# Kernel tuning notes

Hardware: AMD Instinct MI355X
Metric: run time of the kernel (lower is better)

The kernel has to match this reference:

```python
import jax, jax.numpy as jnp
import numpy as np

B, S, D, H = 2, 2048, 1024, 16
HD = D // H
DI = int(8 / 3 * D)  # 2730
EPS = 1e-5


def rmsnorm(x, gamma):
    rms = jnp.sqrt(jnp.mean(x * x, axis=-1, keepdims=True) + EPS)
    return (x / rms) * gamma


def rope(x):
    # x: [B, H, S, HD]; rotate interleaved even/odd pairs, concat halves
    hd = x.shape[-1]
    seq = x.shape[2]
    theta = 1.0 / (10000.0 ** (jnp.arange(0, hd, 2, dtype=jnp.float32) / hd))  # [HD/2]
    ang = jnp.arange(seq, dtype=jnp.float32)[:, None] * theta  # [S, HD/2]
    cos = jnp.cos(ang)[None, None]  # [1,1,S,HD/2]
    sin = jnp.sin(ang)[None, None]
    x1, x2 = x[..., ::2], x[..., 1::2]
    return jnp.concatenate([x1 * cos - x2 * sin, x1 * sin + x2 * cos], axis=-1)


def setup_inputs() -> dict:
    key = jax.random.key(0)
    ks = jax.random.split(key, 8)
    w = lambda k, shape: (jax.random.normal(k, shape, jnp.float32) * 0.02)
    return {
        "x": jax.random.normal(ks[0], (B, S, D), jnp.float32),
        "mask": jnp.tril(jnp.ones((1, 1, S, S), jnp.int32)),  # causal
        "gamma_attn": jnp.ones((D,), jnp.float32),
        "w_qkv": w(ks[1], (3 * D, D)),
        "b_qkv": jnp.zeros((3 * D,), jnp.float32),
        "w_out": w(ks[2], (D, D)),
        "b_out": jnp.zeros((D,), jnp.float32),
        "gamma_ffn": jnp.ones((D,), jnp.float32),
        "w1": w(ks[3], (DI, D)),
        "b1": jnp.zeros((DI,), jnp.float32),
        "w2": w(ks[4], (DI, D)),
        "b2": jnp.zeros((DI,), jnp.float32),
        "w3": w(ks[5], (D, DI)),
        "b3": jnp.zeros((D,), jnp.float32),
    }


def reference(x, mask, gamma_attn, w_qkv, b_qkv, w_out, b_out,
              gamma_ffn, w1, b1, w2, b2, w3, b3):
    batch, seq, d_model = x.shape
    # --- attn norm (pre-norm; residual uses normalized x, matching source) ---
    xn = rmsnorm(x, gamma_attn)
    # --- MHA ---
    qkv = xn @ w_qkv.T + b_qkv  # [B,S,3D]
    q, k, v = jnp.split(qkv, 3, axis=-1)
    q = q.reshape(batch, seq, H, HD).transpose(0, 2, 1, 3)  # [B,H,S,HD]
    k = k.reshape(batch, seq, H, HD).transpose(0, 2, 1, 3)
    v = v.reshape(batch, seq, H, HD).transpose(0, 2, 1, 3)
    q = rope(q)
    k = rope(k)
    scores = jnp.einsum("bhqd,bhkd->bhqk", q, k) / jnp.sqrt(jnp.float32(HD))
    scores = jnp.where(mask == 0, jnp.float32(-jnp.inf), scores)
    attn = jax.nn.softmax(scores, axis=-1)
    out = jnp.einsum("bhqk,bhkd->bhqd", attn, v)
    out = out.transpose(0, 2, 1, 3).reshape(batch, seq, d_model)
    attn_out = out @ w_out.T + b_out
    h = xn + attn_out
    # --- FFN norm + SwiGLU ---
    hn = rmsnorm(h, gamma_ffn)
    gate = jax.nn.silu(hn @ w2.T + b2)
    ff = (hn @ w1.T + b1) * gate
    ffn_out = ff @ w3.T + b3
    return hn + ffn_out
```

## Files before the change

### kernel.cpp

```cpp
#include <hip/hip_runtime.h>

typedef unsigned short u16;
typedef unsigned int u32;
typedef __attribute__((ext_vector_type(8))) short short8;
typedef __attribute__((ext_vector_type(4))) float f32x4;

#define Bt 2
#define St 2048
#define Dm 1024
#define Ht 16
#define HD 64
#define DI 2730
#define DIP 2816
#define DIP2 5632
#define Mrows 4096

typedef const __attribute__((address_space(1))) unsigned char* gp_t;
typedef __attribute__((address_space(3))) unsigned char* lp_t;
#define GLDS16(g, l) __builtin_amdgcn_global_load_lds((gp_t)(g), (lp_t)(l), 16, 0, 0)

__device__ __forceinline__ float bf2f(u16 b){
  union { float f; u32 i; } v; v.i = ((u32)b) << 16; return v.f;
}
__device__ __forceinline__ u16 f2bf(float f){
  union { float f; u32 i; } v; v.f = f;
  u32 u = v.i;
  return (u16)((u + 0x7FFFu + ((u >> 16) & 1u)) >> 16);
}

__global__ __launch_bounds__(256) void prep_k(const float* __restrict__ w_qkv,
                                              const float* __restrict__ w_out,
                                              const float* __restrict__ w1,
                                              const float* __restrict__ w2,
                                              const float* __restrict__ w3,
                                              const float* __restrict__ b1,
                                              const float* __restrict__ b2,
                                              const float* __restrict__ x,
                                              const float* __restrict__ gamma,
                                              u16* __restrict__ w_qkvb,
                                              u16* __restrict__ w_outb,
                                              u16* __restrict__ w12i,
                                              u16* __restrict__ w3b,
                                              float* __restrict__ b12i,
                                              u16* __restrict__ xn)
{
  __shared__ float red[4];
  int bidx = blockIdx.x;
  const int t = threadIdx.x;
  if (bidx < 12288){ const int idx = bidx * 256 + t; w_qkvb[idx] = f2bf(w_qkv[idx]); return; }
  bidx -= 12288;
  if (bidx < 4096){ const int idx = bidx * 256 + t; w_outb[idx] = f2bf(w_out[idx]); return; }
  bidx -= 4096;
  if (bidx < 11264){
    const int idx = bidx * 256 + t;
    const int k = idx >> 10, c = idx & 1023;
    w12i[((size_t)(2 * k)) * 1024 + c] = (k < DI) ? f2bf(w1[idx]) : (u16)0;
    return;
  }
  bidx -= 11264;
  if (bidx < 11264){
    const int idx = bidx * 256 + t;
    const int k = idx >> 10, c = idx & 1023;
    w12i[((size_t)(2 * k + 1)) * 1024 + c] = (k < DI) ? f2bf(w2[idx]) : (u16)0;
    return;
  }
  bidx -= 11264;
  if (bidx < 11264){
    const int idx = bidx * 256 + t;
    const int k = idx % DIP, n = idx / DIP;
    w3b[idx] = (k < DI) ? f2bf(w3[(size_t)n * DI + k]) : (u16)0;
    return;
  }
  bidx -= 11264;
  if (bidx < 22){
    const int idx = bidx * 256 + t;
    if (idx < DIP2){
      const int k = idx >> 1;
      b12i[idx] = (k < DI) ? ((idx & 1) ? b2[k] : b1[k]) : 0.0f;
    }
    return;
  }
  bidx -= 22;
  {
    const size_t base = (size_t)bidx * Dm + t * 4;
    float4 v = *(const float4*)(x + base);
    float ss = v.x*v.x + v.y*v.y + v.z*v.z + v.w*v.w;
    #pragma unroll
    for (int sh = 1; sh < 64; sh <<= 1) ss += __shfl_xor(ss, sh, 64);
    if ((t & 63) == 0) red[t >> 6] = ss;
    __syncthreads();
    float tot = red[0] + red[1] + red[2] + red[3];
    float rinv = 1.0f / sqrtf(tot * (1.0f / 1024.0f) + 1e-5f);
    float4 gv = *(const float4*)(gamma + t * 4);
    uint2 outp;
    outp.x = (u32)f2bf(v.x * rinv * gv.x) | ((u32)f2bf(v.y * rinv * gv.y) << 16);
    outp.y = (u32)f2bf(v.z * rinv * gv.z) | ((u32)f2bf(v.w * rinv * gv.w) << 16);
    *(uint2*)(xn + base) = outp;
  }
}

__global__ __launch_bounds__(256) void rmsnorm2_k(const u16* xa,
                                                  const u16* __restrict__ xb,
                                                  const float* __restrict__ g,
                                                  u16* o)
{
  __shared__ float red[4];
  const int row = blockIdx.x, t = threadIdx.x;
  const size_t base = (size_t)row * Dm + t * 4;
  uint2 va = *(const uint2*)(xa + base);
  uint2 vb = *(const uint2*)(xb + base);
  float f0 = bf2f((u16)(va.x & 0xffff)) + bf2f((u16)(vb.x & 0xffff));
  float f1 = bf2f((u16)(va.x >> 16))    + bf2f((u16)(vb.x >> 16));
  float f2 = bf2f((u16)(va.y & 0xffff)) + bf2f((u16)(vb.y & 0xffff));
  float f3 = bf2f((u16)(va.y >> 16))    + bf2f((u16)(vb.y >> 16));
  float ss = f0*f0 + f1*f1 + f2*f2 + f3*f3;
  #pragma unroll
  for (int sh = 1; sh < 64; sh <<= 1) ss += __shfl_xor(ss, sh, 64);
  if ((t & 63) == 0) red[t >> 6] = ss;
  __syncthreads();
  float tot = red[0] + red[1] + red[2] + red[3];
  float rinv = 1.0f / sqrtf(tot * (1.0f / 1024.0f) + 1e-5f);
  float4 gv = *(const float4*)(g + t * 4);
  uint2 outp;
  outp.x = (u32)f2bf(f0 * rinv * gv.x) | ((u32)f2bf(f1 * rinv * gv.y) << 16);
  outp.y = (u32)f2bf(f2 * rinv * gv.z) | ((u32)f2bf(f3 * rinv * gv.w) << 16);
  *(uint2*)(o + base) = outp;
}

#define BK 32
template<int RES, int WF>
__global__ __launch_bounds__(256) void gemm_bt(const u16* __restrict__ A,
                                               const u16* __restrict__ Bw,
                                               const float* __restrict__ bias,
                                               const u16* __restrict__ res,
                                               void* __restrict__ Cv,
                                               int N, int K, int lda, int ldc)
{
  __shared__ __align__(16) u16 lA[128 * BK];
  __shared__ __align__(16) u16 lB[128 * BK];
  const int tid = threadIdx.x;
  const int m0 = blockIdx.x * 128;
  const int n0 = blockIdx.y * 128;
  const int wave = tid >> 6, lane = tid & 63;
  const int wm = (wave >> 1) * 64, wn = (wave & 1) * 64;
  const int lm = lane & 15, lq = lane >> 4;

  f32x4 acc[4][4] = {};
  const int rl = lane >> 2, seg = lane & 3;

  const int nk = K / BK;
  for (int kt = 0; kt < nk; ++kt){
    const int k0 = kt * BK;
    __syncthreads();
    #pragma unroll
    for (int i = 0; i < 2; ++i){
      const int ra = wave * 32 + i * 16 + rl;
      const int kc = seg ^ ((ra >> 1) & 3);
      GLDS16(A  + (size_t)(m0 + ra) * lda + k0 + kc * 8, &lA[(wave * 32 + i * 16) * BK]);
      GLDS16(Bw + (size_t)(n0 + ra) * K   + k0 + kc * 8, &lB[(wave * 32 + i * 16) * BK]);
    }
    __syncthreads();
    short8 af[4], bfr[4];
    #pragma unroll
    for (int i = 0; i < 4; ++i){
      int r = wm + i * 16 + lm;
      af[i] = *(const short8*)&lA[r * BK + ((lq ^ ((r >> 1) & 3)) * 8)];
    }
    #pragma unroll
    for (int j = 0; j < 4; ++j){
      int r = wn + j * 16 + lm;
      bfr[j] = *(const short8*)&lB[r * BK + ((lq ^ ((r >> 1) & 3)) * 8)];
    }
    #pragma unroll
    for (int i = 0; i < 4; ++i)
      #pragma unroll
      for (int j = 0; j < 4; ++j)
        acc[i][j] = __builtin_amdgcn_mfma_f32_16x16x32_bf16(af[i], bfr[j], acc[i][j], 0, 0, 0);
  }

  #pragma unroll
  for (int i = 0; i < 4; ++i){
    const int row = m0 + wm + i * 16 + lq * 4;
    #pragma unroll
    for (int j = 0; j < 4; ++j){
      const int col = n0 + wn + j * 16 + lm;
      const float bb = bias[col];
      #pragma unroll
      for (int r = 0; r < 4; ++r){
        float v = acc[i][j][r] + bb;
        if (RES) v += bf2f(res[(size_t)(row + r) * ldc + col]);
        if (WF) ((float*)Cv)[(size_t)(row + r) * ldc + col] = v;
        else    ((u16*)Cv)[(size_t)(row + r) * ldc + col] = f2bf(v);
      }
    }
  }
}

__global__ __launch_bounds__(256) void gemm_ffn(const u16* __restrict__ A,
                                                const u16* __restrict__ Bw,
                                                const float* __restrict__ bias,
                                                u16* __restrict__ ff)
{
  __shared__ __align__(16) u16 lA[128 * BK];
  __shared__ __align__(16) u16 lB[128 * BK];
  const int tid = threadIdx.x;
  const int m0 = blockIdx.x * 128;
  const int n0 = blockIdx.y * 128;
  const int wave = tid >> 6, lane = tid & 63;
  const int wm = (wave >> 1) * 64, wn = (wave & 1) * 64;
  const int lm = lane & 15, lq = lane >> 4;

  f32x4 acc[4][4] = {};
  const int rl = lane >> 2, seg = lane & 3;

  for (int kt = 0; kt < 1024 / BK; ++kt){
    const int k0 = kt * BK;
    __syncthreads();
    #pragma unroll
    for (int i = 0; i < 2; ++i){
      const int ra = wave * 32 + i * 16 + rl;
      const int kc = seg ^ ((ra >> 1) & 3);
      GLDS16(A  + (size_t)(m0 + ra) * 1024 + k0 + kc * 8, &lA[(wave * 32 + i * 16) * BK]);
      GLDS16(Bw + (size_t)(n0 + ra) * 1024 + k0 + kc * 8, &lB[(wave * 32 + i * 16) * BK]);
    }
    __syncthreads();
    short8 af[4], bfr[4];
    #pragma unroll
    for (int i = 0; i < 4; ++i){
      int r = wm + i * 16 + lm;
      af[i] = *(const short8*)&lA[r * BK + ((lq ^ ((r >> 1) & 3)) * 8)];
    }
    #pragma unroll
    for (int j = 0; j < 4; ++j){
      int r = wn + j * 16 + lm;
      bfr[j] = *(const short8*)&lB[r * BK + ((lq ^ ((r >> 1) & 3)) * 8)];
    }
    #pragma unroll
    for (int i = 0; i < 4; ++i)
      #pragma unroll
      for (int j = 0; j < 4; ++j)
        acc[i][j] = __builtin_amdgcn_mfma_f32_16x16x32_bf16(af[i], bfr[j], acc[i][j], 0, 0, 0);
  }

  #pragma unroll
  for (int i = 0; i < 4; ++i){
    const int row = m0 + wm + i * 16 + lq * 4;
    #pragma unroll
    for (int j = 0; j < 4; ++j){
      const int col = n0 + wn + j * 16 + lm;
      const float bb = bias[col];
      const int kcol = col >> 1;
      #pragma unroll
      for (int r = 0; r < 4; ++r){
        float v = acc[i][j][r] + bb;
        float g = __shfl_xor(v, 1, 64);
        if ((lm & 1) == 0){
          float ffv = v * (g / (1.0f + __expf(-g)));
          ff[(size_t)(row + r) * DIP + kcol] = f2bf(ffv);
        }
      }
    }
  }
}

template<int RES, int WF>
__global__ __launch_bounds__(256) void gemm_bt64(const u16* __restrict__ A,
                                                 const u16* __restrict__ Bw,
                                                 const float* __restrict__ bias,
                                                 const u16* __restrict__ res,
                                                 void* __restrict__ Cv,
                                                 int N, int K, int lda, int ldc)
{
  __shared__ __align__(16) u16 lA[128 * BK];
  __shared__ __align__(16) u16 lB[64 * BK];
  const int tid = threadIdx.x;
  const int m0 = blockIdx.x * 128;
  const int n0 = blockIdx.y * 64;
  const int wave = tid >> 6, lane = tid & 63;
  const int wm = wave * 32;
  const int lm = lane & 15, lq = lane >> 4;

  f32x4 acc[2][4] = {};
  const int rl = lane >> 2, seg = lane & 3;

  const int nk = K / BK;
  for (int kt = 0; kt < nk; ++kt){
    const int k0 = kt * BK;
    __syncthreads();
    #pragma unroll
    for (int i = 0; i < 2; ++i){
      const int ra = wave * 32 + i * 16 + rl;
      const int kc = seg ^ ((ra >> 1) & 3);
      GLDS16(A + (size_t)(m0 + ra) * lda + k0 + kc * 8, &lA[(wave * 32 + i * 16) * BK]);
    }
    {
      const int rb = wave * 16 + rl;
      const int kc = seg ^ ((rb >> 1) & 3);
      GLDS16(Bw + (size_t)(n0 + rb) * K + k0 + kc * 8, &lB[(wave * 16) * BK]);
    }
    __syncthreads();
    short8 af[2], bfr[4];
    #pragma unroll
    for (int i = 0; i < 2; ++i){
      int r = wm + i * 16 + lm;
      af[i] = *(const short8*)&lA[r * BK + ((lq ^ ((r >> 1) & 3)) * 8)];
    }
    #pragma unroll
    for (int j = 0; j < 4; ++j){
      int r = j * 16 + lm;
      bfr[j] = *(const short8*)&lB[r * BK + ((lq ^ ((r >> 1) & 3)) * 8)];
    }
    #pragma unroll
    for (int i = 0; i < 2; ++i)
      #pragma unroll
      for (int j = 0; j < 4; ++j)
        acc[i][j] = __builtin_amdgcn_mfma_f32_16x16x32_bf16(af[i], bfr[j], acc[i][j], 0, 0, 0);
  }

  #pragma unroll
  for (int i = 0; i < 2; ++i){
    const int row = m0 + wm + i * 16 + lq * 4;
    #pragma unroll
    for (int j = 0; j < 4; ++j){
      const int col = n0 + j * 16 + lm;
      const float bb = bias[col];
      #pragma unroll
      for (int r = 0; r < 4; ++r){
        float v = acc[i][j][r] + bb;
        if (RES) v += bf2f(res[(size_t)(row + r) * ldc + col]);
        if (WF) ((float*)Cv)[(size_t)(row + r) * ldc + col] = v;
        else    ((u16*)Cv)[(size_t)(row + r) * ldc + col] = f2bf(v);
      }
    }
  }
}

__global__ __launch_bounds__(256) void rv_k(const u16* __restrict__ qkv,
                                            u16* __restrict__ qr,
                                            u16* __restrict__ kr,
                                            u16* __restrict__ vT)
{
  __shared__ u16 tbuf[64][66];
  const int bid = blockIdx.x;
  const int tid = threadIdx.x;
  if (bid < 16384){
    const int g = bid * 4 + (tid >> 6);
    const int d = tid & 63;
    const int h = g & 15, m = g >> 4;
    const int s = m & (St - 1), b = m >> 11;
    const int p = d & 31, hi = d >> 5;
    const float theta = __expf(-(float)p * 0.28782313662425575f);
    const float ang = (float)s * theta;
    const float c = cosf(ang), sn = sinf(ang);
    const u16* base = qkv + (size_t)m * 3072;
    float x1q = bf2f(base[h * 64 + 2 * p]);
    float x2q = bf2f(base[h * 64 + 2 * p + 1]);
    float x1k = bf2f(base[1024 + h * 64 + 2 * p]);
    float x2k = bf2f(base[1024 + h * 64 + 2 * p + 1]);
    float vq = (hi == 0) ? (x1q * c - x2q * sn) : (x1q * sn + x2q * c);
    float vk = (hi == 0) ? (x1k * c - x2k * sn) : (x1k * sn + x2k * c);
    const size_t oidx = ((size_t)(b * 16 + h) * St + s) * 64 + d;
    qr[oidx] = f2bf(vq * 0.125f);
    kr[oidx] = f2bf(vk);
  } else {
    const int vt = bid - 16384;
    const int st = vt & 31, bh = vt >> 5;
    const int b = bh >> 4, h = bh & 15;
    const int c2 = (tid & 31) * 2, rg = tid >> 5;
    #pragma unroll
    for (int it = 0; it < 8; ++it){
      int row = rg + it * 8;
      u32 v = *(const u32*)&qkv[(size_t)(b * St + st * 64 + row) * 3072 + 2048 + h * 64 + c2];
      *(u32*)&tbuf[row][c2] = v;
    }
    __syncthreads();
    const int sl = tid & 63;
    #pragma unroll
    for (int it = 0; it < 16; ++it){
      int d = (tid >> 6) + it * 4;
      vT[((size_t)bh * 64 + d) * St + st * 64 + sl] = tbuf[sl][d];
    }
  }
}

__global__ __launch_bounds__(256) void fattn_k(const u16* __restrict__ qr,
                                               const u16* __restrict__ kr,
                                               const u16* __restrict__ vT,
                                               u16* __restrict__ ctx)
{
  __shared__ __align__(16) u16 lK[64 * 80];
  __shared__ __align__(16) u16 lV[64 * 80];
  __shared__ __align__(16) u16 pP[4][2][16 * 72];

  const int bid = blockIdx.x;
  const int bh = bid & 31;
  const int jj = 15 - (bid >> 5);
  const int qt0 = jj << 7;
  const int tid = threadIdx.x;
  const int wave = tid >> 6, lane = tid & 63;
  const int lm = lane & 15, lq = lane >> 4;

  const u16* Kb = kr + (size_t)bh * St * 64;
  const u16* Vb = vT + (size_t)bh * 64 * St;
  const u16* Qb = qr + ((size_t)bh * St + qt0 + wave * 32) * 64;

  short8 qf[2][2];
  #pragma unroll
  for (int st = 0; st < 2; ++st){
    qf[st][0] = *(const short8*)&Qb[(st * 16 + lm) * 64 + lq * 8];
    qf[st][1] = *(const short8*)&Qb[(st * 16 + lm) * 64 + 32 + lq * 8];
  }

  f32x4 o[2][4] = {};
  float ls[2][4] = {};
  const int kend = qt0 + 128;

  for (int kb = 0; kb < kend; kb += 64){
    __syncthreads();
    #pragma unroll
    for (int p = 0; p < 2; ++p){
      const int idx = p * 256 + tid;
      const int r0 = idx >> 3, seg = idx & 7;
      uint4 kv = *(const uint4*)(Kb + (size_t)(kb + r0) * 64 + seg * 8);
      uint4 vv = *(const uint4*)(Vb + (size_t)r0 * St + kb + seg * 8);
      *(uint4*)&lK[r0 * 80 + seg * 8] = kv;
      *(uint4*)&lV[r0 * 80 + seg * 8] = vv;
    }
    __syncthreads();
    f32x4 sc[2][4];
    #pragma unroll
    for (int nt = 0; nt < 4; ++nt){
      const u16* Krow = &lK[(nt * 16 + lm) * 80];
      short8 kf0 = *(const short8*)&Krow[lq * 8];
      short8 kf1 = *(const short8*)&Krow[32 + lq * 8];
      #pragma unroll
      for (int st = 0; st < 2; ++st){
        f32x4 a = {};
        a = __builtin_amdgcn_mfma_f32_16x16x32_bf16(qf[st][0], kf0, a, 0, 0, 0);
        a = __builtin_amdgcn_mfma_f32_16x16x32_bf16(qf[st][1], kf1, a, 0, 0, 0);
        sc[st][nt] = a;
      }
    }
    #pragma unroll
    for (int st = 0; st < 2; ++st){
      const int minrow = qt0 + wave * 32 + st * 16;
      if (kb + 63 > minrow){
        const int rowb = minrow + lq * 4;
        #pragma unroll
        for (int nt = 0; nt < 4; ++nt){
          const int key = kb + nt * 16 + lm;
          #pragma unroll
          for (int r = 0; r < 4; ++r)
            if (key > rowb + r) sc[st][nt][r] = -1e30f;
        }
      }
    }
    #pragma unroll
    for (int st = 0; st < 2; ++st)
      #pragma unroll
      for (int nt = 0; nt < 4; ++nt)
        #pragma unroll
        for (int r = 0; r < 4; ++r){
          float p = __expf(sc[st][nt][r] - 12.0f);
          ls[st][r] += p;
          pP[wave][st][(lq * 4 + r) * 72 + nt * 16 + lm] = f2bf(p);
        }
    short8 pf[2][2];
    #pragma unroll
    for (int st = 0; st < 2; ++st){
      pf[st][0] = *(const short8*)&pP[wave][st][lm * 72 + lq * 8];
      pf[st][1] = *(const short8*)&pP[wave][st][lm * 72 + 32 + lq * 8];
    }
    #pragma unroll
    for (int ct = 0; ct < 4; ++ct){
      const u16* Vrow = &lV[(ct * 16 + lm) * 80];
      short8 vf0 = *(const short8*)&Vrow[lq * 8];
      short8 vf1 = *(const short8*)&Vrow[32 + lq * 8];
      #pragma unroll
      for (int st = 0; st < 2; ++st){
        o[st][ct] = __builtin_amdgcn_mfma_f32_16x16x32_bf16(pf[st][0], vf0, o[st][ct], 0, 0, 0);
        o[st][ct] = __builtin_amdgcn_mfma_f32_16x16x32_bf16(pf[st][1], vf1, o[st][ct], 0, 0, 0);
      }
    }
  }
  #pragma unroll
  for (int sh = 1; sh < 16; sh <<= 1)
    #pragma unroll
    for (int st = 0; st < 2; ++st)
      #pragma unroll
      for (int r = 0; r < 4; ++r)
        ls[st][r] += __shfl_xor(ls[st][r], sh, 64);
  const int b = bh >> 4, h = bh & 15;
  #pragma unroll
  for (int st = 0; st < 2; ++st)
    #pragma unroll
    for (int r = 0; r < 4; ++r){
      const int s = qt0 + wave * 32 + st * 16 + lq * 4 + r;
      const float inv = 1.0f / ls[st][r];
      #pragma unroll
      for (int ct = 0; ct < 4; ++ct){
        const int d = ct * 16 + lm;
        ctx[((size_t)(b * St + s)) * Dm + h * 64 + d] = f2bf(o[st][ct][r] * inv);
      }
    }
}

extern "C" void kernel_launch(void* const* d_in, const int* in_sizes, int n_in,
                              void* d_out, int out_size, void* d_ws, size_t ws_size,
                              hipStream_t stream) {
  (void)in_sizes; (void)n_in; (void)out_size; (void)ws_size;
  const float* x          = (const float*)d_in[0];
  const float* gamma_attn = (const float*)d_in[2];
  const float* w_qkv      = (const float*)d_in[3];
  const float* b_qkv      = (const float*)d_in[4];
  const float* w_out      = (const float*)d_in[5];
  const float* b_out      = (const float*)d_in[6];
  const float* gamma_ffn  = (const float*)d_in[7];
  const float* w1         = (const float*)d_in[8];
  const float* b1         = (const float*)d_in[9];
  const float* w2         = (const float*)d_in[10];
  const float* b2         = (const float*)d_in[11];
  const float* w3         = (const float*)d_in[12];
  const float* b3         = (const float*)d_in[13];
  float* out = (float*)d_out;
  char* ws = (char*)d_ws;

  u16* w_qkvb  = (u16*)(ws + 0);
  u16* w_outb  = (u16*)(ws + 6291456);
  u16* w12i    = (u16*)(ws + 8388608);
  u16* w3b     = (u16*)(ws + 19922944);
  float* b12i  = (float*)(ws + 25690112);
  u16* xn      = (u16*)(ws + 25712640);
  u16* hn      = xn;
  u16* qkv     = (u16*)(ws + 34101248);
  u16* ctx     = (u16*)(ws + 34101248);
  u16* att     = (u16*)(ws + 42489856);
  u16* ff      = (u16*)(ws + 34101248);
  u16* qr      = (u16*)(ws + 59267072);
  u16* kr      = (u16*)(ws + 67655680);
  u16* vT      = (u16*)(ws + 76044288);

  dim3 blk(256);
  prep_k<<<54294, blk, 0, stream>>>(w_qkv, w_out, w1, w2, w3, b1, b2, x, gamma_attn,
                                    w_qkvb, w_outb, w12i, w3b, b12i, xn);
  gemm_bt<0,0><<<dim3(32, 24), blk, 0, stream>>>(xn, w_qkvb, b_qkv, nullptr, qkv, 3072, 1024, 1024, 3072);
  rv_k<<<17408, blk, 0, stream>>>(qkv, qr, kr, vT);
  fattn_k<<<512, blk, 0, stream>>>(qr, kr, vT, ctx);
  gemm_bt64<0,0><<<dim3(32, 16), blk, 0, stream>>>(ctx, w_outb, b_out, nullptr, att, 1024, 1024, 1024, 1024);
  rmsnorm2_k<<<Mrows, blk, 0, stream>>>(xn, att, gamma_ffn, hn);
  gemm_ffn<<<dim3(32, 44), blk, 0, stream>>>(hn, w12i, b12i, ff);
  gemm_bt64<1,1><<<dim3(32, 16), blk, 0, stream>>>(ff, w3b, b3, hn, out, 1024, DIP, DIP, 1024);
}
```

Before: 397.3 us.

## Double GEMM K-tile to 64 with 8-way swizzle and prefetch attention K/V tiles

All three GEMM kernels move from a K-tile of 32 to 64, which halves the number of barrier pairs per K sweep. The LDS XOR swizzle changes to an 8-chunk pattern, and each loaded tile now feeds two MFMA sub-steps. The attention kernel also prefetches the next K/V tile into registers while the current tile is being computed, so global load latency overlaps with math. The cost is more LDS per block and more registers, which may lower occupancy.

```diff
diff --git a/kernel.cpp b/kernel.cpp
--- a/kernel.cpp
+++ b/kernel.cpp
@@ -127,7 +127,7 @@
   *(uint2*)(o + base) = outp;
 }
 
-#define BK 32
+#define BK 64
 template<int RES, int WF>
 __global__ __launch_bounds__(256) void gemm_bt(const u16* __restrict__ A,
                                                const u16* __restrict__ Bw,
@@ -146,36 +146,39 @@
   const int lm = lane & 15, lq = lane >> 4;
 
   f32x4 acc[4][4] = {};
-  const int rl = lane >> 2, seg = lane & 3;
+  const int rl = lane >> 3, seg = lane & 7;
 
   const int nk = K / BK;
   for (int kt = 0; kt < nk; ++kt){
     const int k0 = kt * BK;
     __syncthreads();
     #pragma unroll
-    for (int i = 0; i < 2; ++i){
-      const int ra = wave * 32 + i * 16 + rl;
-      const int kc = seg ^ ((ra >> 1) & 3);
-      GLDS16(A  + (size_t)(m0 + ra) * lda + k0 + kc * 8, &lA[(wave * 32 + i * 16) * BK]);
-      GLDS16(Bw + (size_t)(n0 + ra) * K   + k0 + kc * 8, &lB[(wave * 32 + i * 16) * BK]);
-    }
-    __syncthreads();
-    short8 af[4], bfr[4];
-    #pragma unroll
     for (int i = 0; i < 4; ++i){
-      int r = wm + i * 16 + lm;
-      af[i] = *(const short8*)&lA[r * BK + ((lq ^ ((r >> 1) & 3)) * 8)];
-    }
-    #pragma unroll
-    for (int j = 0; j < 4; ++j){
-      int r = wn + j * 16 + lm;
-      bfr[j] = *(const short8*)&lB[r * BK + ((lq ^ ((r >> 1) & 3)) * 8)];
-    }
-    #pragma unroll
-    for (int i = 0; i < 4; ++i)
-      #pragma unroll
-      for (int j = 0; j < 4; ++j)
-        acc[i][j] = __builtin_amdgcn_mfma_f32_16x16x32_bf16(af[i], bfr[j], acc[i][j], 0, 0, 0);
+      const int ra = wave * 32 + i * 8 + rl;
+      const int kc = seg ^ (ra & 7);
+      GLDS16(A  + (size_t)(m0 + ra) * lda + k0 + kc * 8, &lA[(wave * 32 + i * 8) * BK]);
+      GLDS16(Bw + (size_t)(n0 + ra) * K   + k0 + kc * 8, &lB[(wave * 32 + i * 8) * BK]);
+    }
+    __syncthreads();
+    #pragma unroll
+    for (int h = 0; h < 2; ++h){
+      short8 af[4], bfr[4];
+      #pragma unroll
+      for (int i = 0; i < 4; ++i){
+        int r = wm + i * 16 + lm;
+        af[i] = *(const short8*)&lA[r * BK + (((h * 4 + lq) ^ (r & 7)) * 8)];
+      }
+      #pragma unroll
+      for (int j = 0; j < 4; ++j){
+        int r = wn + j * 16 + lm;
+        bfr[j] = *(const short8*)&lB[r * BK + (((h * 4 + lq) ^ (r & 7)) * 8)];
+      }
+      #pragma unroll
+      for (int i = 0; i < 4; ++i)
+        #pragma unroll
+        for (int j = 0; j < 4; ++j)
+          acc[i][j] = __builtin_amdgcn_mfma_f32_16x16x32_bf16(af[i], bfr[j], acc[i][j], 0, 0, 0);
+    }
   }
 
   #pragma unroll
@@ -211,35 +214,38 @@
   const int lm = lane & 15, lq = lane >> 4;
 
   f32x4 acc[4][4] = {};
-  const int rl = lane >> 2, seg = lane & 3;
+  const int rl = lane >> 3, seg = lane & 7;
 
   for (int kt = 0; kt < 1024 / BK; ++kt){
     const int k0 = kt * BK;
     __syncthreads();
     #pragma unroll
-    for (int i = 0; i < 2; ++i){
-      const int ra = wave * 32 + i * 16 + rl;
-      const int kc = seg ^ ((ra >> 1) & 3);
-      GLDS16(A  + (size_t)(m0 + ra) * 1024 + k0 + kc * 8, &lA[(wave * 32 + i * 16) * BK]);
-      GLDS16(Bw + (size_t)(n0 + ra) * 1024 + k0 + kc * 8, &lB[(wave * 32 + i * 16) * BK]);
-    }
-    __syncthreads();
-    short8 af[4], bfr[4];
-    #pragma unroll
     for (int i = 0; i < 4; ++i){
-      int r = wm + i * 16 + lm;
-      af[i] = *(const short8*)&lA[r * BK + ((lq ^ ((r >> 1) & 3)) * 8)];
-    }
-    #pragma unroll
-    for (int j = 0; j < 4; ++j){
-      int r = wn + j * 16 + lm;
-      bfr[j] = *(const short8*)&lB[r * BK + ((lq ^ ((r >> 1) & 3)) * 8)];
-    }
-    #pragma unroll
-    for (int i = 0; i < 4; ++i)
-      #pragma unroll
-      for (int j = 0; j < 4; ++j)
-        acc[i][j] = __builtin_amdgcn_mfma_f32_16x16x32_bf16(af[i], bfr[j], acc[i][j], 0, 0, 0);
+      const int ra = wave * 32 + i * 8 + rl;
+      const int kc = seg ^ (ra & 7);
+      GLDS16(A  + (size_t)(m0 + ra) * 1024 + k0 + kc * 8, &lA[(wave * 32 + i * 8) * BK]);
+      GLDS16(Bw + (size_t)(n0 + ra) * 1024 + k0 + kc * 8, &lB[(wave * 32 + i * 8) * BK]);
+    }
+    __syncthreads();
+    #pragma unroll
+    for (int h = 0; h < 2; ++h){
+      short8 af[4], bfr[4];
+      #pragma unroll
+      for (int i = 0; i < 4; ++i){
+        int r = wm + i * 16 + lm;
+        af[i] = *(const short8*)&lA[r * BK + (((h * 4 + lq) ^ (r & 7)) * 8)];
+      }
+      #pragma unroll
+      for (int j = 0; j < 4; ++j){
+        int r = wn + j * 16 + lm;
+        bfr[j] = *(const short8*)&lB[r * BK + (((h * 4 + lq) ^ (r & 7)) * 8)];
+      }
+      #pragma unroll
+      for (int i = 0; i < 4; ++i)
+        #pragma unroll
+        for (int j = 0; j < 4; ++j)
+          acc[i][j] = __builtin_amdgcn_mfma_f32_16x16x32_bf16(af[i], bfr[j], acc[i][j], 0, 0, 0);
+    }
   }
 
   #pragma unroll
@@ -281,40 +287,44 @@
   const int lm = lane & 15, lq = lane >> 4;
 
   f32x4 acc[2][4] = {};
-  const int rl = lane >> 2, seg = lane & 3;
+  const int rl = lane >> 3, seg = lane & 7;
 
   const int nk = K / BK;
   for (int kt = 0; kt < nk; ++kt){
     const int k0 = kt * BK;
     __syncthreads();
     #pragma unroll
+    for (int i = 0; i < 4; ++i){
+      const int ra = wave * 32 + i * 8 + rl;
+      const int kc = seg ^ (ra & 7);
+      GLDS16(A + (size_t)(m0 + ra) * lda + k0 + kc * 8, &lA[(wave * 32 + i * 8) * BK]);
+    }
+    #pragma unroll
     for (int i = 0; i < 2; ++i){
-      const int ra = wave * 32 + i * 16 + rl;
-      const int kc = seg ^ ((ra >> 1) & 3);
-      GLDS16(A + (size_t)(m0 + ra) * lda + k0 + kc * 8, &lA[(wave * 32 + i * 16) * BK]);
-    }
-    {
-      const int rb = wave * 16 + rl;
-      const int kc = seg ^ ((rb >> 1) & 3);
-      GLDS16(Bw + (size_t)(n0 + rb) * K + k0 + kc * 8, &lB[(wave * 16) * BK]);
-    }
-    __syncthreads();
-    short8 af[2], bfr[4];
-    #pragma unroll
-    for (int i = 0; i < 2; ++i){
-      int r = wm + i * 16 + lm;
-      af[i] = *(const short8*)&lA[r * BK + ((lq ^ ((r >> 1) & 3)) * 8)];
-    }
-    #pragma unroll
-    for (int j = 0; j < 4; ++j){
-      int r = j * 16 + lm;
-      bfr[j] = *(const short8*)&lB[r * BK + ((lq ^ ((r >> 1) & 3)) * 8)];
-    }
-    #pragma unroll
-    for (int i = 0; i < 2; ++i)
-      #pragma unroll
-      for (int j = 0; j < 4; ++j)
-        acc[i][j] = __builtin_amdgcn_mfma_f32_16x16x32_bf16(af[i], bfr[j], acc[i][j], 0, 0, 0);
+      const int rb = wave * 16 + i * 8 + rl;
+      const int kc = seg ^ (rb & 7);
+      GLDS16(Bw + (size_t)(n0 + rb) * K + k0 + kc * 8, &lB[(wave * 16 + i * 8) * BK]);
+    }
+    __syncthreads();
+    #pragma unroll
+    for (int h = 0; h < 2; ++h){
+      short8 af[2], bfr[4];
+      #pragma unroll
+      for (int i = 0; i < 2; ++i){
+        int r = wm + i * 16 + lm;
+        af[i] = *(const short8*)&lA[r * BK + (((h * 4 + lq) ^ (r & 7)) * 8)];
+      }
+      #pragma unroll
+      for (int j = 0; j < 4; ++j){
+        int r = j * 16 + lm;
+        bfr[j] = *(const short8*)&lB[r * BK + (((h * 4 + lq) ^ (r & 7)) * 8)];
+      }
+      #pragma unroll
+      for (int i = 0; i < 2; ++i)
+        #pragma unroll
+        for (int j = 0; j < 4; ++j)
+          acc[i][j] = __builtin_amdgcn_mfma_f32_16x16x32_bf16(af[i], bfr[j], acc[i][j], 0, 0, 0);
+    }
   }
 
   #pragma unroll
@@ -415,18 +425,34 @@
   float ls[2][4] = {};
   const int kend = qt0 + 128;
 
+  uint4 kpre[2], vpre[2];
+  #pragma unroll
+  for (int p = 0; p < 2; ++p){
+    const int idx = p * 256 + tid;
+    const int r0 = idx >> 3, sg = idx & 7;
+    kpre[p] = *(const uint4*)(Kb + (size_t)r0 * 64 + sg * 8);
+    vpre[p] = *(const uint4*)(Vb + (size_t)r0 * St + sg * 8);
+  }
+
   for (int kb = 0; kb < kend; kb += 64){
     __syncthreads();
     #pragma unroll
     for (int p = 0; p < 2; ++p){
       const int idx = p * 256 + tid;
-      const int r0 = idx >> 3, seg = idx & 7;
-      uint4 kv = *(const uint4*)(Kb + (size_t)(kb + r0) * 64 + seg * 8);
-      uint4 vv = *(const uint4*)(Vb + (size_t)r0 * St + kb + seg * 8);
-      *(uint4*)&lK[r0 * 80 + seg * 8] = kv;
-      *(uint4*)&lV[r0 * 80 + seg * 8] = vv;
-    }
-    __syncthreads();
+      const int r0 = idx >> 3, sg = idx & 7;
+      *(uint4*)&lK[r0 * 80 + sg * 8] = kpre[p];
+      *(uint4*)&lV[r0 * 80 + sg * 8] = vpre[p];
+    }
+    __syncthreads();
+    if (kb + 64 < kend){
+      #pragma unroll
+      for (int p = 0; p < 2; ++p){
+        const int idx = p * 256 + tid;
+        const int r0 = idx >> 3, sg = idx & 7;
+        kpre[p] = *(const uint4*)(Kb + (size_t)(kb + 64 + r0) * 64 + sg * 8);
+        vpre[p] = *(const uint4*)(Vb + (size_t)r0 * St + kb + 64 + sg * 8);
+      }
+    }
     f32x4 sc[2][4];
     #pragma unroll
     for (int nt = 0; nt < 4; ++nt){
```

New measurement: 420.6 us. +5.9%, slower.
